# Performance work log

Measured on AMD Instinct MI355X. Metric: run time of the kernel, lower is better.

The kernel has to match this reference:

```python
import jax, jax.numpy as jnp
import numpy as np


def _cheby_stack(xt, degree):
    # Note: this layer uses T1 = 2*tanh(x) (non-standard), recurrence T_n = 2*xt*T_{n-1} - T_{n-2}
    Ts = [jnp.ones_like(xt)]
    if degree > 0:
        Ts.append(2.0 * xt)
    for n in range(2, degree + 1):
        Ts.append(2.0 * xt * Ts[-1] - Ts[-2])
    return jnp.stack(Ts, axis=2)  # (b, p, n)


def _kan_layer(x, W, tW):
    deg = tW.shape[-1] - 1
    cheby = _cheby_stack(jnp.tanh(x), deg)  # (b, p, n)
    # Fused form of einsum('bpn,qpn->bqp') then einsum('bqp,qp->bq');
    # XLA contracts (tW*W) first, avoiding the huge (b,q,p) intermediate.
    return jnp.einsum('bpn,qpn,qp->bq', cheby, tW, W)


def _cheby_gelu(x, degree=5):
    # Here T1 = tanh(x) (standard), then GeLU(exact) of stacked basis, summed.
    xt = jnp.tanh(x)
    Ts = [jnp.ones_like(xt), xt]
    for n in range(2, degree + 1):
        Ts.append(2.0 * xt * Ts[-1] - Ts[-2])
    st = jnp.stack(Ts, axis=-1)
    return jax.nn.gelu(st, approximate=False).sum(axis=-1)


def setup_inputs() -> dict:
    key = jax.random.key(0)
    ks = jax.random.split(key, 12)
    batch, in_dim, mid, out_dim, deg = 131072, 8, 128, 1, 8
    nfeat = 32
    d = {}
    d['x'] = jax.random.normal(ks[0], (batch, in_dim), jnp.float32)
    d['B'] = jax.random.normal(ks[1], (in_dim, nfeat), jnp.float32)  # scale=1.0
    dims = [(mid, 2 * nfeat), (mid, mid), (mid, mid), (mid, mid), (out_dim, mid)]
    for i, (q, p) in enumerate(dims):
        std_W = np.sqrt(5.0 / (p + q)).astype(np.float32)
        std_tW = np.float32(1.0 / (deg + 1))
        d[f'W{i}'] = std_W * jax.random.normal(ks[2 + 2 * i], (q, p), jnp.float32)
        d[f'tW{i}'] = 0.1 + std_tW * jax.random.normal(ks[3 + 2 * i], (q, p, deg + 1), jnp.float32)
    return d


def reference(x, B, W0, tW0, W1, tW1, W2, tW2, W3, tW3, W4, tW4):
    # FourierFeatures
    proj = (2.0 * jnp.pi) * (x @ B)
    h = jnp.concatenate([jnp.sin(proj), jnp.cos(proj)], axis=-1)  # (b, 64)
    # KAN layers; dropout_prob=0.0 (eval) -> identity. Middle layers get residual
    h = _kan_layer(h, W0, tW0)
    h = _kan_layer(h, W1, tW1) + h
    h = _kan_layer(h, W2, tW2) + h
    h = _kan_layer(h, W3, tW3) + h
    h = _kan_layer(h, W4, tW4)  # (b, 1)
    return _cheby_gelu(h, degree=5)
```

## Files before the change

### kernel.cpp

```cpp
#include <hip/hip_runtime.h>

#define TPB 256

typedef _Float16 f16x8 __attribute__((ext_vector_type(8)));
typedef __fp16 h16x2 __attribute__((ext_vector_type(2)));
typedef float f32x4 __attribute__((ext_vector_type(4)));

static constexpr int WT_L0 = 0;
static constexpr int WT_L1 = 65536;
static constexpr int WT_L2 = 196608;
static constexpr int WT_L3 = 327680;
static constexpr int WT_END = 458752;
static constexpr int F32_BASE = WT_END;
static constexpr int MST = 132;

__device__ __forceinline__ float fast_tanh2(float x) {
  float e = __expf(2.0f * x);
  return fmaf(-4.0f, __builtin_amdgcn_rcpf(e + 1.0f), 2.0f);
}
__device__ __forceinline__ float gelu_exact(float v) {
  return 0.5f * v * (1.0f + erff(v * 0.70710678f));
}

__global__ void fuse_w_f16(const float* __restrict__ W, const float* __restrict__ tW,
                           _Float16* __restrict__ out_hi, _Float16* __restrict__ out_lo,
                           int P, int total, int sbits) {
  int i = blockIdx.x * 256 + threadIdx.x;
  if (i >= total) return;
  int j = i & 7, q = (i >> 3) & 15, g = (i >> 7) & 3, t = (i >> 9) & 7;
  int s = (i >> 12) & ((1 << sbits) - 1);
  int n1 = i >> (12 + sbits);
  int p = s * 32 + g * 8 + j;
  int qg = t * 16 + q;
  float v = tW[(qg * P + p) * 9 + (n1 + 1)] * W[qg * P + p];
  _Float16 hi = (_Float16)v;
  out_hi[i] = hi;
  out_lo[i] = (_Float16)(v - (float)hi);
}
__global__ void fuse_bias(const float* __restrict__ W, const float* __restrict__ tW,
                          float* __restrict__ bias, int P, int Q) {
  int q = blockIdx.x * 64 + threadIdx.x;
  if (q >= Q) return;
  float s = 0.0f;
  for (int p = 0; p < P; ++p) s += tW[(q * P + p) * 9] * W[q * P + p];
  bias[q] = s;
}
__global__ void fuse_w4(const float* __restrict__ W, const float* __restrict__ tW,
                        float* __restrict__ out) {
  int i = blockIdx.x * 128 + threadIdx.x;
  if (i >= 1152) return;
  out[i] = tW[i] * W[i / 9];
}

template <int S, bool RES>
__device__ __forceinline__ void layer22(const float* __restrict__ mT,
                                        const _Float16* __restrict__ wt_hi,
                                        const _Float16* __restrict__ wt_lo,
                                        const float* __restrict__ biasL,
                                        f32x4 (&acc)[2][4], int l, int wr, int wc) {
  const int c15 = l & 15, g = l >> 4;
#pragma unroll
  for (int qt = 0; qt < 4; ++qt) {
    float bv = biasL[wc * 64 + qt * 16 + c15];
#pragma unroll
    for (int rtl = 0; rtl < 2; ++rtl)
#pragma unroll
      for (int j = 0; j < 4; ++j) {
        if (RES) acc[rtl][qt][j] += bv; else acc[rtl][qt][j] = bv;
      }
  }
  const _Float16* bh_base = wt_hi + wc * 2048 + l * 8;
  const _Float16* bl_base = wt_lo + wc * 2048 + l * 8;
  float mv[2][8], up[2][8], uc[2][8];
#pragma unroll 1
  for (int k = 0; k < 8 * S; ++k) {
    int s = k >> 3, n1 = k & 7;
    size_t toff = (size_t)(n1 * S + s) * 4096;
    f16x8 bh[4], bl[4];
#pragma unroll
    for (int qt = 0; qt < 4; ++qt) {
      bh[qt] = *(const f16x8*)(bh_base + toff + qt * 512);
      bl[qt] = *(const f16x8*)(bl_base + toff + qt * 512);
    }
    if (n1 == 0) {
#pragma unroll
      for (int rtl = 0; rtl < 2; ++rtl) {
        const f32x4* mp = (const f32x4*)(mT + (wr * 32 + rtl * 16 + c15) * MST +
                                         s * 32 + g * 8);
        f32x4 a = mp[0], b = mp[1];
#pragma unroll
        for (int i = 0; i < 4; ++i) { mv[rtl][i] = a[i]; mv[rtl][4 + i] = b[i]; }
#pragma unroll
        for (int i = 0; i < 8; ++i) { up[rtl][i] = 1.0f; uc[rtl][i] = mv[rtl][i]; }
      }
    } else {
#pragma unroll
      for (int rtl = 0; rtl < 2; ++rtl)
#pragma unroll
        for (int i = 0; i < 8; ++i) {
          float u = fmaf(mv[rtl][i], uc[rtl][i], -up[rtl][i]);
          up[rtl][i] = uc[rtl][i];
          uc[rtl][i] = u;
        }
    }
    f16x8 afh[2], afl[2];
#pragma unroll
    for (int rtl = 0; rtl < 2; ++rtl) {
      union UU { h16x2 h2[4]; f16x8 v; } uh, ul;
#pragma unroll
      for (int ii = 0; ii < 4; ++ii) {
        float v0 = uc[rtl][2 * ii], v1 = uc[rtl][2 * ii + 1];
        h16x2 h = __builtin_amdgcn_cvt_pkrtz(v0, v1);
        uh.h2[ii] = h;
        ul.h2[ii] = __builtin_amdgcn_cvt_pkrtz(v0 - (float)h[0], v1 - (float)h[1]);
      }
      afh[rtl] = uh.v;
      afl[rtl] = ul.v;
    }
    __builtin_amdgcn_s_setprio(1);
#pragma unroll
    for (int qt = 0; qt < 4; ++qt)
#pragma unroll
      for (int rtl = 0; rtl < 2; ++rtl)
        acc[rtl][qt] = __builtin_amdgcn_mfma_f32_16x16x32_f16(afh[rtl], bh[qt],
                                                              acc[rtl][qt], 0, 0, 0);
#pragma unroll
    for (int qt = 0; qt < 4; ++qt)
#pragma unroll
      for (int rtl = 0; rtl < 2; ++rtl)
        acc[rtl][qt] = __builtin_amdgcn_mfma_f32_16x16x32_f16(afl[rtl], bh[qt],
                                                              acc[rtl][qt], 0, 0, 0);
#pragma unroll
    for (int qt = 0; qt < 4; ++qt)
#pragma unroll
      for (int rtl = 0; rtl < 2; ++rtl)
        acc[rtl][qt] = __builtin_amdgcn_mfma_f32_16x16x32_f16(afh[rtl], bl[qt],
                                                              acc[rtl][qt], 0, 0, 0);
    __builtin_amdgcn_s_setprio(0);
  }
}

__device__ __forceinline__ void write_m(float* __restrict__ mT,
                                        const f32x4 (&acc)[2][4], int l, int wr, int wc) {
  const int c15 = l & 15, g = l >> 4;
#pragma unroll
  for (int rtl = 0; rtl < 2; ++rtl)
#pragma unroll
    for (int qt = 0; qt < 4; ++qt)
#pragma unroll
      for (int j = 0; j < 4; ++j) {
        int row = wr * 32 + rtl * 16 + g * 4 + j;
        int col = wc * 64 + qt * 16 + c15;
        mT[row * MST + col] = fast_tanh2(acc[rtl][qt][j]);
      }
}

__global__ void __launch_bounds__(TPB, 3)
kan_mfma(const float* __restrict__ x, const float* __restrict__ Bm,
         const _Float16* __restrict__ wt_hi, const _Float16* __restrict__ wt_lo,
         const float* __restrict__ bias, const float* __restrict__ w4,
         float* __restrict__ out) {
  __shared__ float mT[64 * MST];
  int tid = threadIdx.x;
  int l = tid & 63;
  int w = tid >> 6;
  int wr = w >> 1, wc = w & 1;
  int row0 = blockIdx.x * 64;

  {
    const float4* xp = (const float4*)(x + (size_t)(row0 + l) * 8);
    float4 a = xp[0], c4 = xp[1];
    float xv[8] = {a.x, a.y, a.z, a.w, c4.x, c4.y, c4.z, c4.w};
#pragma unroll
    for (int jj = 0; jj < 8; ++jj) {
      int j = w * 8 + jj;
      float pr = 0.0f;
#pragma unroll
      for (int k = 0; k < 8; ++k) pr = fmaf(xv[k], Bm[k * 32 + j], pr);
      float ang = 6.2831853071795864f * pr;
      float sv, cv;
      sincosf(ang, &sv, &cv);
      mT[l * MST + j] = fast_tanh2(sv);
      mT[l * MST + 32 + j] = fast_tanh2(cv);
    }
  }
  __syncthreads();

  f32x4 acc[2][4];
  layer22<2, false>(mT, wt_hi + WT_L0, wt_lo + WT_L0, bias + 0, acc, l, wr, wc);
  __syncthreads();
  write_m(mT, acc, l, wr, wc);
  __syncthreads();
  layer22<4, true>(mT, wt_hi + WT_L1, wt_lo + WT_L1, bias + 128, acc, l, wr, wc);
  __syncthreads();
  write_m(mT, acc, l, wr, wc);
  __syncthreads();
  layer22<4, true>(mT, wt_hi + WT_L2, wt_lo + WT_L2, bias + 256, acc, l, wr, wc);
  __syncthreads();
  write_m(mT, acc, l, wr, wc);
  __syncthreads();
  layer22<4, true>(mT, wt_hi + WT_L3, wt_lo + WT_L3, bias + 384, acc, l, wr, wc);
  __syncthreads();
  write_m(mT, acc, l, wr, wc);
  __syncthreads();

  {
    int r16 = l & 15, pq = l >> 4;
    int r = w * 16 + r16;
    const float* w4h = w4 + pq * 32 * 9;
    float part = 0.0f;
#pragma unroll 4
    for (int pp = 0; pp < 32; ++pp) {
      float mm = mT[r * MST + pq * 32 + pp];
      const float* wp = w4h + pp * 9;
      part += wp[0];
      part = fmaf(mm, wp[1], part);
      float u2 = 1.0f, u1 = mm;
#pragma unroll
      for (int n = 2; n < 9; ++n) {
        float u = fmaf(mm, u1, -u2);
        u2 = u1;
        u1 = u;
        part = fmaf(u, wp[n], part);
      }
    }
    part += __shfl_xor(part, 16);
    part += __shfl_xor(part, 32);
    if (l < 16) {
      float v = part;
      float t = 0.5f * fast_tanh2(v);
      float m2 = t + t;
      float tm2 = 1.0f, tm1 = t;
      float y = gelu_exact(1.0f) + gelu_exact(t);
#pragma unroll
      for (int n = 2; n <= 5; ++n) {
        float tn = fmaf(m2, tm1, -tm2);
        tm2 = tm1;
        tm1 = tn;
        y += gelu_exact(tn);
      }
      out[row0 + r] = y;
    }
  }
}

extern "C" void kernel_launch(void* const* d_in, const int* in_sizes, int n_in,
                              void* d_out, int out_size, void* d_ws, size_t ws_size,
                              hipStream_t stream) {
  const float* x   = (const float*)d_in[0];
  const float* Bm  = (const float*)d_in[1];
  const float* W0  = (const float*)d_in[2];
  const float* tW0 = (const float*)d_in[3];
  const float* W1  = (const float*)d_in[4];
  const float* tW1 = (const float*)d_in[5];
  const float* W2  = (const float*)d_in[6];
  const float* tW2 = (const float*)d_in[7];
  const float* W3  = (const float*)d_in[8];
  const float* tW3 = (const float*)d_in[9];
  const float* W4  = (const float*)d_in[10];
  const float* tW4 = (const float*)d_in[11];

  _Float16* wt_hi = (_Float16*)d_ws;
  _Float16* wt_lo = wt_hi + WT_END;
  float* fws = (float*)d_ws + F32_BASE;
  float* bias = fws;
  float* w4 = fws + 512;

  fuse_w_f16<<<65536 / 256, 256, 0, stream>>>(W0, tW0, wt_hi + WT_L0, wt_lo + WT_L0, 64, 65536, 1);
  fuse_w_f16<<<131072 / 256, 256, 0, stream>>>(W1, tW1, wt_hi + WT_L1, wt_lo + WT_L1, 128, 131072, 2);
  fuse_w_f16<<<131072 / 256, 256, 0, stream>>>(W2, tW2, wt_hi + WT_L2, wt_lo + WT_L2, 128, 131072, 2);
  fuse_w_f16<<<131072 / 256, 256, 0, stream>>>(W3, tW3, wt_hi + WT_L3, wt_lo + WT_L3, 128, 131072, 2);
  fuse_bias<<<2, 64, 0, stream>>>(W0, tW0, bias + 0, 64, 128);
  fuse_bias<<<2, 64, 0, stream>>>(W1, tW1, bias + 128, 128, 128);
  fuse_bias<<<2, 64, 0, stream>>>(W2, tW2, bias + 256, 128, 128);
  fuse_bias<<<2, 64, 0, stream>>>(W3, tW3, bias + 384, 128, 128);
  fuse_w4<<<9, 128, 0, stream>>>(W4, tW4, w4);

  kan_mfma<<<131072 / 64, TPB, 0, stream>>>(x, Bm, wt_hi, wt_lo, bias, w4, (float*)d_out);
}
```

Measured before the change: 435.7 us.

## Stage fused weights through double-buffered LDS via global_load_lds

Each weight chunk (hi and lo halves) is now loaded cooperatively into a double-buffered LDS region with direct global-to-LDS loads, prefetching the next k-step while the current one computes. Previously every wave pulled its own fragments from global/L2 memory, so both column-halves of waves duplicated traffic. The change adds a block-wide barrier every k iteration and 32KB more LDS, and occupancy hint drops from 3 to 2 blocks per CU.

```diff
diff --git a/kernel.cpp b/kernel.cpp
--- a/kernel.cpp
+++ b/kernel.cpp
@@ -20,6 +20,11 @@
 }
 __device__ __forceinline__ float gelu_exact(float v) {
   return 0.5f * v * (1.0f + erff(v * 0.70710678f));
+}
+__device__ __forceinline__ void gload_lds16(const void* g, void* l) {
+  __builtin_amdgcn_global_load_lds(
+      (const __attribute__((address_space(1))) unsigned int*)g,
+      (__attribute__((address_space(3))) unsigned int*)l, 16, 0, 0);
 }
 
 __global__ void fuse_w_f16(const float* __restrict__ W, const float* __restrict__ tW,
@@ -53,11 +58,13 @@
 }
 
 template <int S, bool RES>
-__device__ __forceinline__ void layer22(const float* __restrict__ mT,
-                                        const _Float16* __restrict__ wt_hi,
-                                        const _Float16* __restrict__ wt_lo,
-                                        const float* __restrict__ biasL,
-                                        f32x4 (&acc)[2][4], int l, int wr, int wc) {
+__device__ __forceinline__ void layer_lds(const float* __restrict__ mT,
+                                          char* __restrict__ bb,
+                                          const _Float16* __restrict__ wt_hi,
+                                          const _Float16* __restrict__ wt_lo,
+                                          const float* __restrict__ biasL,
+                                          f32x4 (&acc)[2][4], int l, int w,
+                                          int wr, int wc) {
   const int c15 = l & 15, g = l >> 4;
 #pragma unroll
   for (int qt = 0; qt < 4; ++qt) {
@@ -69,18 +76,33 @@
         if (RES) acc[rtl][qt][j] += bv; else acc[rtl][qt][j] = bv;
       }
   }
-  const _Float16* bh_base = wt_hi + wc * 2048 + l * 8;
-  const _Float16* bl_base = wt_lo + wc * 2048 + l * 8;
+  const char* wsrc0 = (w < 2 ? (const char*)wt_hi + (size_t)w * 4096
+                             : (const char*)wt_lo + (size_t)(w - 2) * 4096) + l * 16;
+  char* wdst0 = bb + w * 4096;
   float mv[2][8], up[2][8], uc[2][8];
+
+#pragma unroll
+  for (int i = 0; i < 4; ++i) gload_lds16(wsrc0 + i * 1024, wdst0 + i * 1024);
+  __syncthreads();
+
 #pragma unroll 1
   for (int k = 0; k < 8 * S; ++k) {
     int s = k >> 3, n1 = k & 7;
-    size_t toff = (size_t)(n1 * S + s) * 4096;
+    int cur = k & 1;
+    if (k + 1 < 8 * S) {
+      int s2 = (k + 1) >> 3, n12 = (k + 1) & 7;
+      size_t ck2 = (size_t)(n12 * S + s2) * 8192;
+      const char* src = wsrc0 + ck2;
+      char* dst = wdst0 + (cur ^ 1) * 16384;
+#pragma unroll
+      for (int i = 0; i < 4; ++i) gload_lds16(src + i * 1024, dst + i * 1024);
+    }
+    const char* rb = bb + cur * 16384 + wc * 4096 + l * 16;
     f16x8 bh[4], bl[4];
 #pragma unroll
     for (int qt = 0; qt < 4; ++qt) {
-      bh[qt] = *(const f16x8*)(bh_base + toff + qt * 512);
-      bl[qt] = *(const f16x8*)(bl_base + toff + qt * 512);
+      bh[qt] = *(const f16x8*)(rb + qt * 1024);
+      bl[qt] = *(const f16x8*)(rb + 8192 + qt * 1024);
     }
     if (n1 == 0) {
 #pragma unroll
@@ -137,6 +159,7 @@
         acc[rtl][qt] = __builtin_amdgcn_mfma_f32_16x16x32_f16(afh[rtl], bl[qt],
                                                               acc[rtl][qt], 0, 0, 0);
     __builtin_amdgcn_s_setprio(0);
+    __syncthreads();
   }
 }
 
@@ -155,12 +178,13 @@
       }
 }
 
-__global__ void __launch_bounds__(TPB, 3)
+__global__ void __launch_bounds__(TPB, 2)
 kan_mfma(const float* __restrict__ x, const float* __restrict__ Bm,
          const _Float16* __restrict__ wt_hi, const _Float16* __restrict__ wt_lo,
          const float* __restrict__ bias, const float* __restrict__ w4,
          float* __restrict__ out) {
   __shared__ float mT[64 * MST];
+  __shared__ __align__(16) char bbuf[2][16384];
   int tid = threadIdx.x;
   int l = tid & 63;
   int w = tid >> 6;
@@ -187,20 +211,16 @@
   __syncthreads();
 
   f32x4 acc[2][4];
-  layer22<2, false>(mT, wt_hi + WT_L0, wt_lo + WT_L0, bias + 0, acc, l, wr, wc);
-  __syncthreads();
+  layer_lds<2, false>(mT, &bbuf[0][0], wt_hi + WT_L0, wt_lo + WT_L0, bias + 0, acc, l, w, wr, wc);
   write_m(mT, acc, l, wr, wc);
   __syncthreads();
-  layer22<4, true>(mT, wt_hi + WT_L1, wt_lo + WT_L1, bias + 128, acc, l, wr, wc);
-  __syncthreads();
+  layer_lds<4, true>(mT, &bbuf[0][0], wt_hi + WT_L1, wt_lo + WT_L1, bias + 128, acc, l, w, wr, wc);
   write_m(mT, acc, l, wr, wc);
   __syncthreads();
-  layer22<4, true>(mT, wt_hi + WT_L2, wt_lo + WT_L2, bias + 256, acc, l, wr, wc);
-  __syncthreads();
+  layer_lds<4, true>(mT, &bbuf[0][0], wt_hi + WT_L2, wt_lo + WT_L2, bias + 256, acc, l, w, wr, wc);
   write_m(mT, acc, l, wr, wc);
   __syncthreads();
-  layer22<4, true>(mT, wt_hi + WT_L3, wt_lo + WT_L3, bias + 384, acc, l, wr, wc);
-  __syncthreads();
+  layer_lds<4, true>(mT, &bbuf[0][0], wt_hi + WT_L3, wt_lo + WT_L3, bias + 384, acc, l, w, wr, wc);
   write_m(mT, acc, l, wr, wc);
   __syncthreads();
 
```

Result: slower. 487.6 us (+11.9%).

## Use two waves per block with 64x64 per-wave tiles to halve weight loads

Applied to the files above, without the earlier changes.

Each 64-row block now runs with 2 waves instead of 4, and each wave covers all 64 rows times 64 output columns (4x4 MFMA tiles) instead of 32x64. Every weight fragment loaded from global/L2 now feeds twice as many MFMAs, which halves per-block weight traffic. The final output layer is reorganized so each wave handles half the inputs, with the partial sums combined through shared memory. The cost is much higher register pressure (64 accumulator floats plus three 4x8 recurrence arrays), lower launch bounds occupancy (2), and fewer waves available to hide latency.

```diff
diff --git a/kernel.cpp b/kernel.cpp
--- a/kernel.cpp
+++ b/kernel.cpp
@@ -1,6 +1,6 @@
 #include <hip/hip_runtime.h>
 
-#define TPB 256
+#define TPB 128
 
 typedef _Float16 f16x8 __attribute__((ext_vector_type(8)));
 typedef __fp16 h16x2 __attribute__((ext_vector_type(2)));
@@ -53,25 +53,25 @@
 }
 
 template <int S, bool RES>
-__device__ __forceinline__ void layer22(const float* __restrict__ mT,
+__device__ __forceinline__ void layer44(const float* __restrict__ mT,
                                         const _Float16* __restrict__ wt_hi,
                                         const _Float16* __restrict__ wt_lo,
                                         const float* __restrict__ biasL,
-                                        f32x4 (&acc)[2][4], int l, int wr, int wc) {
+                                        f32x4 (&acc)[4][4], int l, int wv) {
   const int c15 = l & 15, g = l >> 4;
 #pragma unroll
   for (int qt = 0; qt < 4; ++qt) {
-    float bv = biasL[wc * 64 + qt * 16 + c15];
-#pragma unroll
-    for (int rtl = 0; rtl < 2; ++rtl)
+    float bv = biasL[wv * 64 + qt * 16 + c15];
+#pragma unroll
+    for (int rt = 0; rt < 4; ++rt)
 #pragma unroll
       for (int j = 0; j < 4; ++j) {
-        if (RES) acc[rtl][qt][j] += bv; else acc[rtl][qt][j] = bv;
-      }
-  }
-  const _Float16* bh_base = wt_hi + wc * 2048 + l * 8;
-  const _Float16* bl_base = wt_lo + wc * 2048 + l * 8;
-  float mv[2][8], up[2][8], uc[2][8];
+        if (RES) acc[rt][qt][j] += bv; else acc[rt][qt][j] = bv;
+      }
+  }
+  const _Float16* bh_base = wt_hi + wv * 2048 + l * 8;
+  const _Float16* bl_base = wt_lo + wv * 2048 + l * 8;
+  float mv[4][8], up[4][8], uc[4][8];
 #pragma unroll 1
   for (int k = 0; k < 8 * S; ++k) {
     int s = k >> 3, n1 = k & 7;
@@ -84,87 +84,86 @@
     }
     if (n1 == 0) {
 #pragma unroll
-      for (int rtl = 0; rtl < 2; ++rtl) {
-        const f32x4* mp = (const f32x4*)(mT + (wr * 32 + rtl * 16 + c15) * MST +
-                                         s * 32 + g * 8);
+      for (int rt = 0; rt < 4; ++rt) {
+        const f32x4* mp = (const f32x4*)(mT + (rt * 16 + c15) * MST + s * 32 + g * 8);
         f32x4 a = mp[0], b = mp[1];
 #pragma unroll
-        for (int i = 0; i < 4; ++i) { mv[rtl][i] = a[i]; mv[rtl][4 + i] = b[i]; }
-#pragma unroll
-        for (int i = 0; i < 8; ++i) { up[rtl][i] = 1.0f; uc[rtl][i] = mv[rtl][i]; }
+        for (int i = 0; i < 4; ++i) { mv[rt][i] = a[i]; mv[rt][4 + i] = b[i]; }
+#pragma unroll
+        for (int i = 0; i < 8; ++i) { up[rt][i] = 1.0f; uc[rt][i] = mv[rt][i]; }
       }
     } else {
 #pragma unroll
-      for (int rtl = 0; rtl < 2; ++rtl)
+      for (int rt = 0; rt < 4; ++rt)
 #pragma unroll
         for (int i = 0; i < 8; ++i) {
-          float u = fmaf(mv[rtl][i], uc[rtl][i], -up[rtl][i]);
-          up[rtl][i] = uc[rtl][i];
-          uc[rtl][i] = u;
+          float u = fmaf(mv[rt][i], uc[rt][i], -up[rt][i]);
+          up[rt][i] = uc[rt][i];
+          uc[rt][i] = u;
         }
     }
-    f16x8 afh[2], afl[2];
-#pragma unroll
-    for (int rtl = 0; rtl < 2; ++rtl) {
+    f16x8 afh[4], afl[4];
+#pragma unroll
+    for (int rt = 0; rt < 4; ++rt) {
       union UU { h16x2 h2[4]; f16x8 v; } uh, ul;
 #pragma unroll
       for (int ii = 0; ii < 4; ++ii) {
-        float v0 = uc[rtl][2 * ii], v1 = uc[rtl][2 * ii + 1];
+        float v0 = uc[rt][2 * ii], v1 = uc[rt][2 * ii + 1];
         h16x2 h = __builtin_amdgcn_cvt_pkrtz(v0, v1);
         uh.h2[ii] = h;
         ul.h2[ii] = __builtin_amdgcn_cvt_pkrtz(v0 - (float)h[0], v1 - (float)h[1]);
       }
-      afh[rtl] = uh.v;
-      afl[rtl] = ul.v;
+      afh[rt] = uh.v;
+      afl[rt] = ul.v;
     }
     __builtin_amdgcn_s_setprio(1);
 #pragma unroll
     for (int qt = 0; qt < 4; ++qt)
 #pragma unroll
-      for (int rtl = 0; rtl < 2; ++rtl)
-        acc[rtl][qt] = __builtin_amdgcn_mfma_f32_16x16x32_f16(afh[rtl], bh[qt],
-                                                              acc[rtl][qt], 0, 0, 0);
-#pragma unroll
-    for (int qt = 0; qt < 4; ++qt)
-#pragma unroll
-      for (int rtl = 0; rtl < 2; ++rtl)
-        acc[rtl][qt] = __builtin_amdgcn_mfma_f32_16x16x32_f16(afl[rtl], bh[qt],
-                                                              acc[rtl][qt], 0, 0, 0);
-#pragma unroll
-    for (int qt = 0; qt < 4; ++qt)
-#pragma unroll
-      for (int rtl = 0; rtl < 2; ++rtl)
-        acc[rtl][qt] = __builtin_amdgcn_mfma_f32_16x16x32_f16(afh[rtl], bl[qt],
-                                                              acc[rtl][qt], 0, 0, 0);
+      for (int rt = 0; rt < 4; ++rt)
+        acc[rt][qt] = __builtin_amdgcn_mfma_f32_16x16x32_f16(afh[rt], bh[qt],
+                                                             acc[rt][qt], 0, 0, 0);
+#pragma unroll
+    for (int qt = 0; qt < 4; ++qt)
+#pragma unroll
+      for (int rt = 0; rt < 4; ++rt)
+        acc[rt][qt] = __builtin_amdgcn_mfma_f32_16x16x32_f16(afl[rt], bh[qt],
+                                                             acc[rt][qt], 0, 0, 0);
+#pragma unroll
+    for (int qt = 0; qt < 4; ++qt)
+#pragma unroll
+      for (int rt = 0; rt < 4; ++rt)
+        acc[rt][qt] = __builtin_amdgcn_mfma_f32_16x16x32_f16(afh[rt], bl[qt],
+                                                             acc[rt][qt], 0, 0, 0);
     __builtin_amdgcn_s_setprio(0);
   }
 }
 
 __device__ __forceinline__ void write_m(float* __restrict__ mT,
-                                        const f32x4 (&acc)[2][4], int l, int wr, int wc) {
+                                        const f32x4 (&acc)[4][4], int l, int wv) {
   const int c15 = l & 15, g = l >> 4;
 #pragma unroll
-  for (int rtl = 0; rtl < 2; ++rtl)
+  for (int rt = 0; rt < 4; ++rt)
 #pragma unroll
     for (int qt = 0; qt < 4; ++qt)
 #pragma unroll
       for (int j = 0; j < 4; ++j) {
-        int row = wr * 32 + rtl * 16 + g * 4 + j;
-        int col = wc * 64 + qt * 16 + c15;
-        mT[row * MST + col] = fast_tanh2(acc[rtl][qt][j]);
-      }
-}
-
-__global__ void __launch_bounds__(TPB, 3)
+        int row = rt * 16 + g * 4 + j;
+        int col = wv * 64 + qt * 16 + c15;
+        mT[row * MST + col] = fast_tanh2(acc[rt][qt][j]);
+      }
+}
+
+__global__ void __launch_bounds__(TPB, 2)
 kan_mfma(const float* __restrict__ x, const float* __restrict__ Bm,
          const _Float16* __restrict__ wt_hi, const _Float16* __restrict__ wt_lo,
          const float* __restrict__ bias, const float* __restrict__ w4,
          float* __restrict__ out) {
   __shared__ float mT[64 * MST];
+  __shared__ float xb[64];
   int tid = threadIdx.x;
   int l = tid & 63;
-  int w = tid >> 6;
-  int wr = w >> 1, wc = w & 1;
+  int wv = tid >> 6;
   int row0 = blockIdx.x * 64;
 
   {
@@ -172,8 +171,8 @@
     float4 a = xp[0], c4 = xp[1];
     float xv[8] = {a.x, a.y, a.z, a.w, c4.x, c4.y, c4.z, c4.w};
 #pragma unroll
-    for (int jj = 0; jj < 8; ++jj) {
-      int j = w * 8 + jj;
+    for (int jj = 0; jj < 16; ++jj) {
+      int j = wv * 16 + jj;
       float pr = 0.0f;
 #pragma unroll
       for (int k = 0; k < 8; ++k) pr = fmaf(xv[k], Bm[k * 32 + j], pr);
@@ -186,32 +185,31 @@
   }
   __syncthreads();
 
-  f32x4 acc[2][4];
-  layer22<2, false>(mT, wt_hi + WT_L0, wt_lo + WT_L0, bias + 0, acc, l, wr, wc);
-  __syncthreads();
-  write_m(mT, acc, l, wr, wc);
-  __syncthreads();
-  layer22<4, true>(mT, wt_hi + WT_L1, wt_lo + WT_L1, bias + 128, acc, l, wr, wc);
-  __syncthreads();
-  write_m(mT, acc, l, wr, wc);
-  __syncthreads();
-  layer22<4, true>(mT, wt_hi + WT_L2, wt_lo + WT_L2, bias + 256, acc, l, wr, wc);
-  __syncthreads();
-  write_m(mT, acc, l, wr, wc);
-  __syncthreads();
-  layer22<4, true>(mT, wt_hi + WT_L3, wt_lo + WT_L3, bias + 384, acc, l, wr, wc);
-  __syncthreads();
-  write_m(mT, acc, l, wr, wc);
+  f32x4 acc[4][4];
+  layer44<2, false>(mT, wt_hi + WT_L0, wt_lo + WT_L0, bias + 0, acc, l, wv);
+  __syncthreads();
+  write_m(mT, acc, l, wv);
+  __syncthreads();
+  layer44<4, true>(mT, wt_hi + WT_L1, wt_lo + WT_L1, bias + 128, acc, l, wv);
+  __syncthreads();
+  write_m(mT, acc, l, wv);
+  __syncthreads();
+  layer44<4, true>(mT, wt_hi + WT_L2, wt_lo + WT_L2, bias + 256, acc, l, wv);
+  __syncthreads();
+  write_m(mT, acc, l, wv);
+  __syncthreads();
+  layer44<4, true>(mT, wt_hi + WT_L3, wt_lo + WT_L3, bias + 384, acc, l, wv);
+  __syncthreads();
+  write_m(mT, acc, l, wv);
   __syncthreads();
 
   {
-    int r16 = l & 15, pq = l >> 4;
-    int r = w * 16 + r16;
-    const float* w4h = w4 + pq * 32 * 9;
+    const float* w4h = w4 + wv * 64 * 9;
+    const float* mrow = mT + l * MST + wv * 64;
     float part = 0.0f;
 #pragma unroll 4
-    for (int pp = 0; pp < 32; ++pp) {
-      float mm = mT[r * MST + pq * 32 + pp];
+    for (int pp = 0; pp < 64; ++pp) {
+      float mm = mrow[pp];
       const float* wp = w4h + pp * 9;
       part += wp[0];
       part = fmaf(mm, wp[1], part);
@@ -224,10 +222,10 @@
         part = fmaf(u, wp[n], part);
       }
     }
-    part += __shfl_xor(part, 16);
-    part += __shfl_xor(part, 32);
-    if (l < 16) {
-      float v = part;
+    if (wv == 1) xb[l] = part;
+    __syncthreads();
+    if (wv == 0) {
+      float v = part + xb[l];
       float t = 0.5f * fast_tanh2(v);
       float m2 = t + t;
       float tm2 = 1.0f, tm1 = t;
@@ -239,7 +237,7 @@
         tm1 = tn;
         y += gelu_exact(tn);
       }
-      out[row0 + r] = y;
+      out[row0 + l] = y;
     }
   }
 }
```

After: 500.0 us. 14.7% more time.
